# Optimization experiments

Measured on AMD Instinct MI355X. Metric: run time of the kernel, lower is better.

## Reference

```python
import jax, jax.numpy as jnp
import numpy as np

IN_FEATURES = 512
OUT_FEATURES = 512
BATCH = 1024


def setup_inputs() -> dict:
    key = jax.random.key(0)
    k_x, k_bw, k_ww, k_sc, k_tr, k_b = jax.random.split(key, 6)
    std = 1.0 / np.sqrt(IN_FEATURES)
    x = jax.random.normal(k_x, (BATCH, IN_FEATURES), dtype=jnp.float32)
    base_weight = jax.random.uniform(k_bw, (OUT_FEATURES, IN_FEATURES), jnp.float32, -std, std)
    wavelet_weights = jax.random.uniform(k_ww, (OUT_FEATURES, IN_FEATURES), jnp.float32, -std, std)
    # scale initialized to ones in the module; perturb slightly (kept positive) for a non-degenerate test
    scale = jnp.exp(0.1 * jax.random.normal(k_sc, (OUT_FEATURES, IN_FEATURES), dtype=jnp.float32))
    translation = 0.1 * jax.random.normal(k_tr, (OUT_FEATURES, IN_FEATURES), dtype=jnp.float32)
    bias = jax.random.uniform(k_b, (OUT_FEATURES,), jnp.float32, -std, std)
    return {"x": x, "base_weight": base_weight, "wavelet_weights": wavelet_weights,
            "scale": scale, "translation": translation, "bias": bias}


def reference(x, base_weight, wavelet_weights, scale, translation, bias):
    # base branch: SiLU then linear
    base_out = jnp.einsum("bi,oi->bo", jax.nn.silu(x), base_weight)
    # wavelet branch: broadcast x to (batch, out, in)
    xs = (x[:, None, :] - translation[None, :, :]) / scale[None, :, :]  # (B, O, I)
    wavelet = (xs * xs - 1.0) * jnp.exp(-0.5 * xs * xs)  # mexican hat
    wavelet_out = jnp.einsum("boi,oi->bo", wavelet, wavelet_weights)
    return base_out + wavelet_out + bias
```

## Files before the change

kernel.cpp:

```cpp
#include <hip/hip_runtime.h>


constexpr int IN_F  = 512;
constexpr int OUT_F = 512;
constexpr int BATCH = 1024;
constexpr int BT = 128, OT = 64;
constexpr int KS = 8;
constexpr int KR = IN_F / KS;
constexpr int IT = 16;
constexpr int PITCH = IT + 4;
constexpr int HP = IT + 4;
constexpr int LP = OT + 1;
constexpr int NCH = KR / IT;
constexpr int BO  = BATCH * OUT_F;

#define LOG2E 1.44269504088897f
#define C2f   (-0.72134752044448f)
#define NC2f  ( 0.72134752044448f)
#define RQf   (-0.84083003f)

typedef float v2f   __attribute__((ext_vector_type(2)));
typedef float f32x4 __attribute__((ext_vector_type(4)));
typedef _Float16 half4 __attribute__((ext_vector_type(4)));

__device__ __forceinline__ float fexp2(float v) { return __builtin_amdgcn_exp2f(v); }
__device__ __forceinline__ float frcp(float v)  { return __builtin_amdgcn_rcpf(v); }
__device__ __forceinline__ v2f pkfma(v2f a, v2f b, v2f c) {
  return __builtin_elementwise_fma(a, b, c);
}
__device__ __forceinline__ float fsilu(float v) {
  return v * frcp(1.f + fexp2(v * -LOG2E));
}

__global__ __launch_bounds__(256, 2)
void wkan_main(const float* __restrict__ x, const float* __restrict__ basew,
               const float* __restrict__ wavew, const float* __restrict__ scale,
               const float* __restrict__ transl, const float* __restrict__ bias,
               float* __restrict__ partial, float* __restrict__ out, int use_ws)
{
  __shared__ float lx [BT * PITCH];
  __shared__ float la [OT * PITCH];
  __shared__ float lm [OT * PITCH];
  __shared__ float ln [OT * PITCH];
  __shared__ float lq [OT * PITCH];
  __shared__ _Float16 hx [BT * HP];
  __shared__ _Float16 hb [OT * HP];
  __shared__ float lout[BT * LP];

  const int tid = threadIdx.x;
  const int b0 = blockIdx.x * BT;
  const int o0 = blockIdx.y * OT;
  const int ks = blockIdx.z;
  const int k0 = ks * KR;

  const int srow = tid >> 2;
  const int sc4  = (tid & 3) * 4;
  const int lofs = srow * PITCH + sc4;
  const int hofs = srow * HP + sc4;

  const int to = tid & 15;
  const int tb = tid >> 4;

  const int lane = tid & 63;
  const int wid  = tid >> 6;
  const int frow = lane & 15;
  const int kgrp = (lane >> 4) * 4;

  v2f zz; zz.x = 0.f; zz.y = 0.f;
  v2f acc[8][4];
#pragma unroll
  for (int r = 0; r < 8; ++r)
#pragma unroll
    for (int c = 0; c < 4; ++c) acc[r][c] = zz;

  f32x4 accb[2][4];
#pragma unroll
  for (int mt = 0; mt < 2; ++mt)
#pragma unroll
    for (int nt = 0; nt < 4; ++nt) accb[mt][nt] = (f32x4)0.f;

  float4 xv0, xv1, sv, tv, wv, bv;
  {
    const int g = k0 + sc4;
    xv0 = *(const float4*)(x      + (size_t)(b0 + srow)      * IN_F + g);
    xv1 = *(const float4*)(x      + (size_t)(b0 + srow + 64) * IN_F + g);
    sv  = *(const float4*)(scale  + (size_t)(o0 + srow) * IN_F + g);
    tv  = *(const float4*)(transl + (size_t)(o0 + srow) * IN_F + g);
    wv  = *(const float4*)(wavew  + (size_t)(o0 + srow) * IN_F + g);
    bv  = *(const float4*)(basew  + (size_t)(o0 + srow) * IN_F + g);
  }

  for (int kc = 0; kc < NCH; ++kc) {
    if (kc) __syncthreads();
    {
      float4 sx0, sx1;
      sx0.x = fsilu(xv0.x); sx0.y = fsilu(xv0.y); sx0.z = fsilu(xv0.z); sx0.w = fsilu(xv0.w);
      sx1.x = fsilu(xv1.x); sx1.y = fsilu(xv1.y); sx1.z = fsilu(xv1.z); sx1.w = fsilu(xv1.w);
      *(float4*)(lx + lofs) = xv0;
      *(float4*)(lx + lofs + 64 * PITCH) = xv1;
      half4 h0, h1;
      h0[0] = (_Float16)sx0.x; h0[1] = (_Float16)sx0.y;
      h0[2] = (_Float16)sx0.z; h0[3] = (_Float16)sx0.w;
      h1[0] = (_Float16)sx1.x; h1[1] = (_Float16)sx1.y;
      h1[2] = (_Float16)sx1.z; h1[3] = (_Float16)sx1.w;
      *(half4*)(hx + hofs) = h0;
      *(half4*)(hx + hofs + 64 * HP) = h1;

      float4 av, mv, nv;
      {
        float a2, a2t;
        a2 = C2f * frcp(sv.x * sv.x); a2t = a2 * tv.x;
        av.x = a2; mv.x = -2.f * a2t; nv.x = fmaf(a2t, tv.x, NC2f);
        a2 = C2f * frcp(sv.y * sv.y); a2t = a2 * tv.y;
        av.y = a2; mv.y = -2.f * a2t; nv.y = fmaf(a2t, tv.y, NC2f);
        a2 = C2f * frcp(sv.z * sv.z); a2t = a2 * tv.z;
        av.z = a2; mv.z = -2.f * a2t; nv.z = fmaf(a2t, tv.z, NC2f);
        a2 = C2f * frcp(sv.w * sv.w); a2t = a2 * tv.w;
        av.w = a2; mv.w = -2.f * a2t; nv.w = fmaf(a2t, tv.w, NC2f);
      }
      *(float4*)(la + lofs) = av;
      *(float4*)(lm + lofs) = mv;
      *(float4*)(ln + lofs) = nv;

      float4 qv;
      qv.x = wv.x * RQf; qv.y = wv.y * RQf; qv.z = wv.z * RQf; qv.w = wv.w * RQf;
      *(float4*)(lq + lofs) = qv;

      half4 hbv;
      hbv[0] = (_Float16)bv.x; hbv[1] = (_Float16)bv.y;
      hbv[2] = (_Float16)bv.z; hbv[3] = (_Float16)bv.w;
      *(half4*)(hb + hofs) = hbv;
    }
    __syncthreads();

    if (kc + 1 < NCH) {
      const int g = k0 + (kc + 1) * IT + sc4;
      xv0 = *(const float4*)(x      + (size_t)(b0 + srow)      * IN_F + g);
      xv1 = *(const float4*)(x      + (size_t)(b0 + srow + 64) * IN_F + g);
      sv  = *(const float4*)(scale  + (size_t)(o0 + srow) * IN_F + g);
      tv  = *(const float4*)(transl + (size_t)(o0 + srow) * IN_F + g);
      wv  = *(const float4*)(wavew  + (size_t)(o0 + srow) * IN_F + g);
      bv  = *(const float4*)(basew  + (size_t)(o0 + srow) * IN_F + g);
    }

    {
      half4 af0 = *(const half4*)(hx + (wid * 32 +      frow) * HP + kgrp);
      half4 af1 = *(const half4*)(hx + (wid * 32 + 16 + frow) * HP + kgrp);
#pragma unroll
      for (int nt = 0; nt < 4; ++nt) {
        half4 bf = *(const half4*)(hb + (nt * 16 + frow) * HP + kgrp);
        accb[0][nt] = __builtin_amdgcn_mfma_f32_16x16x16f16(af0, bf, accb[0][nt], 0, 0, 0);
        accb[1][nt] = __builtin_amdgcn_mfma_f32_16x16x16f16(af1, bf, accb[1][nt], 0, 0, 0);
      }
    }

    for (int ii = 0; ii < IT; ii += 4) {
      float4 xr[8], x2[8];
#pragma unroll
      for (int r = 0; r < 8; ++r) {
        const int row = (tb + 16 * r) * PITCH + ii;
        xr[r] = *(const float4*)(lx + row);
        x2[r].x = xr[r].x * xr[r].x;
        x2[r].y = xr[r].y * xr[r].y;
        x2[r].z = xr[r].z * xr[r].z;
        x2[r].w = xr[r].w * xr[r].w;
      }
#pragma unroll
      for (int c = 0; c < 4; ++c) {
        const int orow = (to + 16 * c) * PITCH + ii;
        float4 A = *(const float4*)(la + orow);
        float4 M = *(const float4*)(lm + orow);
        float4 N = *(const float4*)(ln + orow);
        float4 Q = *(const float4*)(lq + orow);
        v2f Al = {A.x, A.y}, Ah = {A.z, A.w};
        v2f Ml = {M.x, M.y}, Mh = {M.z, M.w};
        v2f Nl = {N.x, N.y}, Nh = {N.z, N.w};
        v2f Ql = {Q.x, Q.y}, Qh = {Q.z, Q.w};
#pragma unroll
        for (int r = 0; r < 8; ++r) {
          v2f xl  = {xr[r].x, xr[r].y}, xh  = {xr[r].z, xr[r].w};
          v2f x2l = {x2[r].x, x2[r].y}, x2h = {x2[r].z, x2[r].w};
          v2f p, e, gg;
          p = pkfma(Al, x2l, pkfma(Ml, xl, Nl));
          e.x = fexp2(p.x); e.y = fexp2(p.y);
          gg = p * Ql;
          acc[r][c] = pkfma(gg, e, acc[r][c]);
          p = pkfma(Ah, x2h, pkfma(Mh, xh, Nh));
          e.x = fexp2(p.x); e.y = fexp2(p.y);
          gg = p * Qh;
          acc[r][c] = pkfma(gg, e, acc[r][c]);
        }
      }
    }
  }

#pragma unroll
  for (int mt = 0; mt < 2; ++mt)
#pragma unroll
    for (int nt = 0; nt < 4; ++nt)
#pragma unroll
      for (int i = 0; i < 4; ++i)
        lout[(wid * 32 + mt * 16 + (lane >> 4) * 4 + i) * LP + nt * 16 + frow]
            = accb[mt][nt][i];
  __syncthreads();

#pragma unroll
  for (int r = 0; r < 8; ++r) {
    const int br = b0 + tb + 16 * r;
#pragma unroll
    for (int c = 0; c < 4; ++c) {
      const int oc = o0 + to + 16 * c;
      float res = acc[r][c].x + acc[r][c].y
                + lout[(tb + 16 * r) * LP + to + 16 * c];
      if (use_ws) {
        partial[(size_t)ks * BO + (size_t)br * OUT_F + oc] = res;
      } else {
        if (ks == 0) res += bias[oc];
        atomicAdd(out + (size_t)br * OUT_F + oc, res);
      }
    }
  }
}

__global__ __launch_bounds__(256)
void wkan_reduce(const float* __restrict__ partial, const float* __restrict__ bias,
                 float* __restrict__ out)
{
  const int i4 = (blockIdx.x * 256 + threadIdx.x) * 4;
  float4 r = *(const float4*)(bias + (i4 & (OUT_F - 1)));
#pragma unroll
  for (int k = 0; k < KS; ++k) {
    float4 a = *(const float4*)(partial + (size_t)k * BO + i4);
    r.x += a.x; r.y += a.y; r.z += a.z; r.w += a.w;
  }
  *(float4*)(out + i4) = r;
}

extern "C" void kernel_launch(void* const* d_in, const int* in_sizes, int n_in,
                              void* d_out, int out_size, void* d_ws, size_t ws_size,
                              hipStream_t stream) {
  const float* x  = (const float*)d_in[0];
  const float* bw = (const float*)d_in[1];
  const float* ww = (const float*)d_in[2];
  const float* sc = (const float*)d_in[3];
  const float* tr = (const float*)d_in[4];
  const float* bi = (const float*)d_in[5];
  float* out = (float*)d_out;

  const int use_ws = ws_size >= (size_t)KS * BO * sizeof(float) ? 1 : 0;
  if (!use_ws) {
    hipMemsetAsync(d_out, 0, (size_t)out_size * sizeof(float), stream);
  }
  dim3 grid(BATCH / BT, OUT_F / OT, KS);
  wkan_main<<<grid, dim3(256), 0, stream>>>(x, bw, ww, sc, tr, bi,
                                            (float*)d_ws, out, use_ws);
  if (use_ws) {
    wkan_reduce<<<dim3(BO / 1024), dim3(256), 0, stream>>>((const float*)d_ws, bi, out);
  }
}
```

Baseline: 111.1 us.

## Halve output tile, union shared memory, and drop register prefetch

Cuts the output tile per block from 64 to 32, so each thread keeps half as many wavelet and MFMA accumulators. It also packs all shared buffers into one array with the output staging buffer reusing the same space. Global loads now happen inside each chunk instead of being prefetched into registers, and only half the threads stage the per-output parameters. The polynomial is evaluated in Horner form so no x² values are kept. The aim is lower register and LDS pressure for higher occupancy, at the cost of lost load/compute overlap and more blocks that each restage x.

```diff
diff --git a/kernel.cpp b/kernel.cpp
--- a/kernel.cpp
+++ b/kernel.cpp
@@ -4,7 +4,7 @@
 constexpr int IN_F  = 512;
 constexpr int OUT_F = 512;
 constexpr int BATCH = 1024;
-constexpr int BT = 128, OT = 64;
+constexpr int BT = 128, OT = 32;
 constexpr int KS = 8;
 constexpr int KR = IN_F / KS;
 constexpr int IT = 16;
@@ -32,20 +32,23 @@
   return v * frcp(1.f + fexp2(v * -LOG2E));
 }
 
+constexpr int SMEM_F = 6720;
+
 __global__ __launch_bounds__(256, 2)
 void wkan_main(const float* __restrict__ x, const float* __restrict__ basew,
                const float* __restrict__ wavew, const float* __restrict__ scale,
                const float* __restrict__ transl, const float* __restrict__ bias,
                float* __restrict__ partial, float* __restrict__ out, int use_ws)
 {
-  __shared__ float lx [BT * PITCH];
-  __shared__ float la [OT * PITCH];
-  __shared__ float lm [OT * PITCH];
-  __shared__ float ln [OT * PITCH];
-  __shared__ float lq [OT * PITCH];
-  __shared__ _Float16 hx [BT * HP];
-  __shared__ _Float16 hb [OT * HP];
-  __shared__ float lout[BT * LP];
+  __shared__ float smem[SMEM_F];
+  float* lx = smem;
+  float* la = smem + 2560;
+  float* lm = smem + 3200;
+  float* ln = smem + 3840;
+  float* lq = smem + 4480;
+  _Float16* hx = (_Float16*)(smem + 5120);
+  _Float16* hb = (_Float16*)(smem + 6400);
+  float* lout = smem;
 
   const int tid = threadIdx.x;
   const int b0 = blockIdx.x * BT;
@@ -57,6 +60,8 @@
   const int sc4  = (tid & 3) * 4;
   const int lofs = srow * PITCH + sc4;
   const int hofs = srow * HP + sc4;
+  const int prow = tid >> 2;
+  const int pofs = prow * PITCH + sc4;
 
   const int to = tid & 15;
   const int tb = tid >> 4;
@@ -67,32 +72,24 @@
   const int kgrp = (lane >> 4) * 4;
 
   v2f zz; zz.x = 0.f; zz.y = 0.f;
-  v2f acc[8][4];
+  v2f acc[8][2];
 #pragma unroll
   for (int r = 0; r < 8; ++r)
 #pragma unroll
-    for (int c = 0; c < 4; ++c) acc[r][c] = zz;
-
-  f32x4 accb[2][4];
+    for (int c = 0; c < 2; ++c) acc[r][c] = zz;
+
+  f32x4 accb[2][2];
 #pragma unroll
   for (int mt = 0; mt < 2; ++mt)
 #pragma unroll
-    for (int nt = 0; nt < 4; ++nt) accb[mt][nt] = (f32x4)0.f;
-
-  float4 xv0, xv1, sv, tv, wv, bv;
-  {
-    const int g = k0 + sc4;
-    xv0 = *(const float4*)(x      + (size_t)(b0 + srow)      * IN_F + g);
-    xv1 = *(const float4*)(x      + (size_t)(b0 + srow + 64) * IN_F + g);
-    sv  = *(const float4*)(scale  + (size_t)(o0 + srow) * IN_F + g);
-    tv  = *(const float4*)(transl + (size_t)(o0 + srow) * IN_F + g);
-    wv  = *(const float4*)(wavew  + (size_t)(o0 + srow) * IN_F + g);
-    bv  = *(const float4*)(basew  + (size_t)(o0 + srow) * IN_F + g);
-  }
+    for (int nt = 0; nt < 2; ++nt) accb[mt][nt] = (f32x4)0.f;
 
   for (int kc = 0; kc < NCH; ++kc) {
+    const int g = k0 + kc * IT + sc4;
     if (kc) __syncthreads();
     {
+      float4 xv0 = *(const float4*)(x + (size_t)(b0 + srow)      * IN_F + g);
+      float4 xv1 = *(const float4*)(x + (size_t)(b0 + srow + 64) * IN_F + g);
       float4 sx0, sx1;
       sx0.x = fsilu(xv0.x); sx0.y = fsilu(xv0.y); sx0.z = fsilu(xv0.z); sx0.w = fsilu(xv0.w);
       sx1.x = fsilu(xv1.x); sx1.y = fsilu(xv1.y); sx1.z = fsilu(xv1.z); sx1.w = fsilu(xv1.w);
@@ -106,67 +103,59 @@
       *(half4*)(hx + hofs) = h0;
       *(half4*)(hx + hofs + 64 * HP) = h1;
 
-      float4 av, mv, nv;
-      {
-        float a2, a2t;
-        a2 = C2f * frcp(sv.x * sv.x); a2t = a2 * tv.x;
-        av.x = a2; mv.x = -2.f * a2t; nv.x = fmaf(a2t, tv.x, NC2f);
-        a2 = C2f * frcp(sv.y * sv.y); a2t = a2 * tv.y;
-        av.y = a2; mv.y = -2.f * a2t; nv.y = fmaf(a2t, tv.y, NC2f);
-        a2 = C2f * frcp(sv.z * sv.z); a2t = a2 * tv.z;
-        av.z = a2; mv.z = -2.f * a2t; nv.z = fmaf(a2t, tv.z, NC2f);
-        a2 = C2f * frcp(sv.w * sv.w); a2t = a2 * tv.w;
-        av.w = a2; mv.w = -2.f * a2t; nv.w = fmaf(a2t, tv.w, NC2f);
-      }
-      *(float4*)(la + lofs) = av;
-      *(float4*)(lm + lofs) = mv;
-      *(float4*)(ln + lofs) = nv;
-
-      float4 qv;
-      qv.x = wv.x * RQf; qv.y = wv.y * RQf; qv.z = wv.z * RQf; qv.w = wv.w * RQf;
-      *(float4*)(lq + lofs) = qv;
-
-      half4 hbv;
-      hbv[0] = (_Float16)bv.x; hbv[1] = (_Float16)bv.y;
-      hbv[2] = (_Float16)bv.z; hbv[3] = (_Float16)bv.w;
-      *(half4*)(hb + hofs) = hbv;
+      if (tid < 128) {
+        float4 sv = *(const float4*)(scale  + (size_t)(o0 + prow) * IN_F + g);
+        float4 tv = *(const float4*)(transl + (size_t)(o0 + prow) * IN_F + g);
+        float4 av, mv, nv;
+        {
+          float a2, a2t;
+          a2 = C2f * frcp(sv.x * sv.x); a2t = a2 * tv.x;
+          av.x = a2; mv.x = -2.f * a2t; nv.x = fmaf(a2t, tv.x, NC2f);
+          a2 = C2f * frcp(sv.y * sv.y); a2t = a2 * tv.y;
+          av.y = a2; mv.y = -2.f * a2t; nv.y = fmaf(a2t, tv.y, NC2f);
+          a2 = C2f * frcp(sv.z * sv.z); a2t = a2 * tv.z;
+          av.z = a2; mv.z = -2.f * a2t; nv.z = fmaf(a2t, tv.z, NC2f);
+          a2 = C2f * frcp(sv.w * sv.w); a2t = a2 * tv.w;
+          av.w = a2; mv.w = -2.f * a2t; nv.w = fmaf(a2t, tv.w, NC2f);
+        }
+        *(float4*)(la + pofs) = av;
+        *(float4*)(lm + pofs) = mv;
+        *(float4*)(ln + pofs) = nv;
+
+        float4 wv = *(const float4*)(wavew + (size_t)(o0 + prow) * IN_F + g);
+        float4 qv;
+        qv.x = wv.x * RQf; qv.y = wv.y * RQf; qv.z = wv.z * RQf; qv.w = wv.w * RQf;
+        *(float4*)(lq + pofs) = qv;
+
+        float4 bv = *(const float4*)(basew + (size_t)(o0 + prow) * IN_F + g);
+        half4 hbv;
+        hbv[0] = (_Float16)bv.x; hbv[1] = (_Float16)bv.y;
+        hbv[2] = (_Float16)bv.z; hbv[3] = (_Float16)bv.w;
+        *(half4*)(hb + pofs) = hbv;
+      }
     }
     __syncthreads();
-
-    if (kc + 1 < NCH) {
-      const int g = k0 + (kc + 1) * IT + sc4;
-      xv0 = *(const float4*)(x      + (size_t)(b0 + srow)      * IN_F + g);
-      xv1 = *(const float4*)(x      + (size_t)(b0 + srow + 64) * IN_F + g);
-      sv  = *(const float4*)(scale  + (size_t)(o0 + srow) * IN_F + g);
-      tv  = *(const float4*)(transl + (size_t)(o0 + srow) * IN_F + g);
-      wv  = *(const float4*)(wavew  + (size_t)(o0 + srow) * IN_F + g);
-      bv  = *(const float4*)(basew  + (size_t)(o0 + srow) * IN_F + g);
-    }
 
     {
       half4 af0 = *(const half4*)(hx + (wid * 32 +      frow) * HP + kgrp);
       half4 af1 = *(const half4*)(hx + (wid * 32 + 16 + frow) * HP + kgrp);
-#pragma unroll
-      for (int nt = 0; nt < 4; ++nt) {
-        half4 bf = *(const half4*)(hb + (nt * 16 + frow) * HP + kgrp);
-        accb[0][nt] = __builtin_amdgcn_mfma_f32_16x16x16f16(af0, bf, accb[0][nt], 0, 0, 0);
-        accb[1][nt] = __builtin_amdgcn_mfma_f32_16x16x16f16(af1, bf, accb[1][nt], 0, 0, 0);
-      }
+      half4 bf0 = *(const half4*)(hb + (       frow) * HP + kgrp);
+      half4 bf1 = *(const half4*)(hb + (16 +   frow) * HP + kgrp);
+      accb[0][0] = __builtin_amdgcn_mfma_f32_16x16x16f16(af0, bf0, accb[0][0], 0, 0, 0);
+      accb[0][1] = __builtin_amdgcn_mfma_f32_16x16x16f16(af0, bf1, accb[0][1], 0, 0, 0);
+      accb[1][0] = __builtin_amdgcn_mfma_f32_16x16x16f16(af1, bf0, accb[1][0], 0, 0, 0);
+      accb[1][1] = __builtin_amdgcn_mfma_f32_16x16x16f16(af1, bf1, accb[1][1], 0, 0, 0);
     }
 
     for (int ii = 0; ii < IT; ii += 4) {
-      float4 xr[8], x2[8];
+      float4 xr[8];
 #pragma unroll
       for (int r = 0; r < 8; ++r) {
         const int row = (tb + 16 * r) * PITCH + ii;
         xr[r] = *(const float4*)(lx + row);
-        x2[r].x = xr[r].x * xr[r].x;
-        x2[r].y = xr[r].y * xr[r].y;
-        x2[r].z = xr[r].z * xr[r].z;
-        x2[r].w = xr[r].w * xr[r].w;
-      }
-#pragma unroll
-      for (int c = 0; c < 4; ++c) {
+      }
+#pragma unroll
+      for (int c = 0; c < 2; ++c) {
         const int orow = (to + 16 * c) * PITCH + ii;
         float4 A = *(const float4*)(la + orow);
         float4 M = *(const float4*)(lm + orow);
@@ -179,13 +168,12 @@
 #pragma unroll
         for (int r = 0; r < 8; ++r) {
           v2f xl  = {xr[r].x, xr[r].y}, xh  = {xr[r].z, xr[r].w};
-          v2f x2l = {x2[r].x, x2[r].y}, x2h = {x2[r].z, x2[r].w};
           v2f p, e, gg;
-          p = pkfma(Al, x2l, pkfma(Ml, xl, Nl));
+          p = pkfma(pkfma(Al, xl, Ml), xl, Nl);
           e.x = fexp2(p.x); e.y = fexp2(p.y);
           gg = p * Ql;
           acc[r][c] = pkfma(gg, e, acc[r][c]);
-          p = pkfma(Ah, x2h, pkfma(Mh, xh, Nh));
+          p = pkfma(pkfma(Ah, xh, Mh), xh, Nh);
           e.x = fexp2(p.x); e.y = fexp2(p.y);
           gg = p * Qh;
           acc[r][c] = pkfma(gg, e, acc[r][c]);
@@ -194,10 +182,11 @@
     }
   }
 
+  __syncthreads();
 #pragma unroll
   for (int mt = 0; mt < 2; ++mt)
 #pragma unroll
-    for (int nt = 0; nt < 4; ++nt)
+    for (int nt = 0; nt < 2; ++nt)
 #pragma unroll
       for (int i = 0; i < 4; ++i)
         lout[(wid * 32 + mt * 16 + (lane >> 4) * 4 + i) * LP + nt * 16 + frow]
@@ -208,7 +197,7 @@
   for (int r = 0; r < 8; ++r) {
     const int br = b0 + tb + 16 * r;
 #pragma unroll
-    for (int c = 0; c < 4; ++c) {
+    for (int c = 0; c < 2; ++c) {
       const int oc = o0 + to + 16 * c;
       float res = acc[r][c].x + acc[r][c].y
                 + lout[(tb + 16 * r) * LP + to + 16 * c];
```

After: 107.6 us. 1.03x faster.
